# Performance work log

Measured on AMD Instinct MI355X. Metric: run time of the kernel, lower is better.

Reference implementation:

```python
import jax, jax.numpy as jnp
import numpy as np

B, T, D, H = 4, 2048, 1024, 16
HD = D // H

def setup_inputs() -> dict:
    key = jax.random.key(0)
    ks = jax.random.split(key, 12)
    s = 0.02
    return {
        "query": jax.random.normal(ks[0], (B, T, D), dtype=jnp.float32),
        "key_": jax.random.normal(ks[1], (B, T, D), dtype=jnp.float32),
        "value": jax.random.normal(ks[2], (B, T, D), dtype=jnp.float32),
        "attention_mask": jnp.zeros((B, T, T), dtype=bool),
        "Wq": jax.random.normal(ks[3], (D, D), dtype=jnp.float32) * s,
        "bq": jnp.zeros((D,), dtype=jnp.float32),
        "Wk": jax.random.normal(ks[4], (D, D), dtype=jnp.float32) * s,
        "bk": jnp.zeros((D,), dtype=jnp.float32),
        "Wv": jax.random.normal(ks[5], (D, D), dtype=jnp.float32) * s,
        "bv": jnp.zeros((D,), dtype=jnp.float32),
        "Wo": jax.random.normal(ks[6], (D, D), dtype=jnp.float32) * s,
        "bo": jnp.zeros((D,), dtype=jnp.float32),
    }

def reference(query, key_, value, attention_mask, Wq, bq, Wk, bk, Wv, bv, Wo, bo):
    scale = 1.0 / jnp.sqrt(jnp.float32(HD))
    # projections (torch Linear: x @ W.T + b), split heads -> [B, H, T, HD]
    q = (query @ Wq.T + bq).reshape(B, T, H, HD).transpose(0, 2, 1, 3)
    k = (key_ @ Wk.T + bk).reshape(B, T, H, HD).transpose(0, 2, 1, 3)
    v = (value @ Wv.T + bv).reshape(B, T, H, HD).transpose(0, 2, 1, 3)
    scores = jnp.einsum('bhqd,bhkd->bhqk', q, k) * scale  # [B,H,T,T]
    mask = attention_mask[:, None, :, :]  # [B,1,T,T], True = masked
    scores = jnp.where(mask, -jnp.inf, scores)
    attn = jax.nn.softmax(scores, axis=-1)
    out = jnp.einsum('bhqk,bhkd->bhqd', attn, v)  # [B,H,T,HD]
    out = out.transpose(0, 2, 1, 3).reshape(B, T, D)
    return out @ Wo.T + bo
```

## Files before the change

kernel.cpp:

```cpp
#include <hip/hip_runtime.h>
#include <hip/hip_bf16.h>
#include <math.h>


typedef short bf16x8 __attribute__((ext_vector_type(8)));
typedef short bf16x4 __attribute__((ext_vector_type(4)));
typedef float f32x4  __attribute__((ext_vector_type(4)));
typedef float f32x16 __attribute__((ext_vector_type(16)));
typedef unsigned u32x4v __attribute__((ext_vector_type(4)));

#define DEV __device__ __forceinline__

DEV short f2bf(float f) {
    union { float f; unsigned u; } x; x.f = f;
    unsigned r = x.u + 0x7fffu + ((x.u >> 16) & 1u);
    return (short)(r >> 16);
}

DEV unsigned cvtpk(float lo, float hi) {
    unsigned r;
    asm("v_cvt_pk_bf16_f32 %0, %1, %2" : "=v"(r) : "v"(lo), "v"(hi));
    return r;
}

DEV void pl32swap(unsigned &a, unsigned &b) {
    asm volatile("v_permlane32_swap_b32 %0, %1" : "+v"(a), "+v"(b));
}

DEV float fexp2(float x) {
    float r;
    asm("v_exp_f32 %0, %1\n\ts_nop 0" : "=v"(r) : "v"(x));
    return r;
}

DEV void gload16(const void* g, void* lds_wave_base) {
    __builtin_amdgcn_global_load_lds(
        (const __attribute__((address_space(1))) void*)g,
        (__attribute__((address_space(3))) void*)lds_wave_base, 16, 0, 0);
}

DEV f32x4 mfma16(bf16x8 a, bf16x8 b, f32x4 c) {
    return __builtin_amdgcn_mfma_f32_16x16x32_bf16(a, b, c, 0, 0, 0);
}
DEV f32x16 mfma32(bf16x8 a, bf16x8 b, f32x16 c) {
    return __builtin_amdgcn_mfma_f32_32x32x16_bf16(a, b, c, 0, 0, 0);
}

__global__ __launch_bounds__(256) void cvt_w4(
    const float* __restrict__ a, const float* __restrict__ b,
    const float* __restrict__ c, const float* __restrict__ d,
    short* __restrict__ oa, short* __restrict__ ob,
    short* __restrict__ oc, short* __restrict__ od) {
    const int sel = blockIdx.x >> 9;
    const float* in = sel == 0 ? a : sel == 1 ? b : sel == 2 ? c : d;
    short* out      = sel == 0 ? oa : sel == 1 ? ob : sel == 2 ? oc : od;
    int i = ((blockIdx.x & 511) * 256 + threadIdx.x) * 8;
    f32x4 x = *(const f32x4*)(in + i);
    f32x4 y = *(const f32x4*)(in + i + 4);
    union { unsigned u[4]; bf16x8 v; } p;
    p.u[0] = cvtpk(x[0], x[1]); p.u[1] = cvtpk(x[2], x[3]);
    p.u[2] = cvtpk(y[0], y[1]); p.u[3] = cvtpk(y[2], y[3]);
    *(bf16x8*)(out + i) = p.v;
}

__global__ __launch_bounds__(256) void gemm_qkv(
    const float* __restrict__ Aq, const float* __restrict__ Ak, const float* __restrict__ Av,
    const short* __restrict__ Wqb, const short* __restrict__ Wkb, const short* __restrict__ Wvb,
    const float* __restrict__ bqp, const float* __restrict__ bkp, const float* __restrict__ bvp,
    short* __restrict__ Qo, short* __restrict__ Ko, short* __restrict__ Vo, float qscale)
{
    __shared__ short Alds[2][4096];
    __shared__ short Blds[2][4096];

    const int t = threadIdx.x, wave = t >> 6, lane = t & 63;
    const int lr = lane & 15, lg = lane >> 4;
    const int raw = blockIdx.x;
    const int wg = (raw & 7) * 192 + (raw >> 3);
    const int sel = wg >> 9, inner = wg & 511;
    const int m0 = (inner >> 3) * 128, n0 = (inner & 7) * 128;
    const int wr = wave >> 1, wc = wave & 1;

    const float* A    = sel == 0 ? Aq  : sel == 1 ? Ak  : Av;
    const short* W    = sel == 0 ? Wqb : sel == 1 ? Wkb : Wvb;
    const float* bias = sel == 0 ? bqp : sel == 1 ? bkp : bvp;

    const int arow = t & 127, kh = t >> 7;
    const float* Asrc = A + (size_t)(m0 + arow) * 1024 + kh * 16;
    const int o0 = t * 16,        kb0 = o0 >> 11, row0 = (o0 >> 4) & 127;
    const int o1 = 4096 + t * 16, kb1 = o1 >> 11, row1 = (o1 >> 4) & 127;
    const short* Ws0 = W + (size_t)(n0 + row0) * 1024 + kb0 * 8;
    const short* Ws1 = W + (size_t)(n0 + row1) * 1024 + kb1 * 8;

    f32x4 ar0, ar1, ar2, ar3;
    auto aload = [&](int k0) {
        ar0 = *(const f32x4*)(Asrc + k0);
        ar1 = *(const f32x4*)(Asrc + k0 + 4);
        ar2 = *(const f32x4*)(Asrc + k0 + 8);
        ar3 = *(const f32x4*)(Asrc + k0 + 12);
    };
    auto awrite = [&](short* dst0) {
        union { unsigned u[4]; bf16x8 v; } p0, p1;
        p0.u[0] = cvtpk(ar0[0], ar0[1]); p0.u[1] = cvtpk(ar0[2], ar0[3]);
        p0.u[2] = cvtpk(ar1[0], ar1[1]); p0.u[3] = cvtpk(ar1[2], ar1[3]);
        p1.u[0] = cvtpk(ar2[0], ar2[1]); p1.u[1] = cvtpk(ar2[2], ar2[3]);
        p1.u[2] = cvtpk(ar3[0], ar3[1]); p1.u[3] = cvtpk(ar3[2], ar3[3]);
        short* dst = dst0 + (kh * 2) * 1024 + arow * 8;
        *(bf16x8*)dst          = p0.v;
        *(bf16x8*)(dst + 1024) = p1.v;
    };
    auto wstage = [&](short* dB, int k0) {
        gload16(Ws0 + k0, (char*)dB + wave * 1024);
        gload16(Ws1 + k0, (char*)dB + 4096 + wave * 1024);
    };

    f32x4 acc[4][4] = {};

    aload(0);
    asm volatile("s_waitcnt vmcnt(0)" ::: "memory");
    awrite(Alds[0]);
    wstage(Blds[0], 0);
    aload(32);

    #pragma unroll 1
    for (int ts = 0; ts < 32; ++ts) {
        const int B = ts & 1;
        if (ts < 31) asm volatile("s_waitcnt vmcnt(4) lgkmcnt(0)" ::: "memory");
        else         asm volatile("s_waitcnt vmcnt(0) lgkmcnt(0)" ::: "memory");
        __builtin_amdgcn_s_barrier();
        bf16x8 af[4], bfr[4];
        #pragma unroll
        for (int mi = 0; mi < 4; mi++)
            af[mi] = *(const bf16x8*)(Alds[B] + lg * 1024 + (wr * 64 + mi * 16 + lr) * 8);
        #pragma unroll
        for (int ni = 0; ni < 4; ni++)
            bfr[ni] = *(const bf16x8*)(Blds[B] + lg * 1024 + (wc * 64 + ni * 16 + lr) * 8);
        if (ts < 31) wstage(Blds[B ^ 1], (ts + 1) * 32);
        #pragma unroll
        for (int mi = 0; mi < 4; mi++)
            #pragma unroll
            for (int ni = 0; ni < 4; ni++)
                acc[mi][ni] = mfma16(af[mi], bfr[ni], acc[mi][ni]);
        if (ts < 31) {
            asm volatile("s_waitcnt vmcnt(2)" ::: "memory");
            awrite(Alds[B ^ 1]);
            if (ts < 30) aload((ts + 2) * 32);
        }
    }

    #pragma unroll
    for (int mi = 0; mi < 4; mi++) {
        #pragma unroll
        for (int ni = 0; ni < 4; ni++) {
            const int n      = n0 + wc * 64 + ni * 16 + lr;
            const int m_base = m0 + wr * 64 + mi * 16 + lg * 4;
            const float bv   = bias[n];
            f32x4 a = acc[mi][ni];
            if (sel == 2) {
                const int bb = m_base >> 11, tt = m_base & 2047;
                bf16x4 p;
                #pragma unroll
                for (int r = 0; r < 4; r++) p[r] = f2bf(a[r] + bv);
                *(bf16x4*)(Vo + (size_t)bb * 2097152 + (size_t)n * 2048 + tt) = p;
            } else {
                short* C = sel ? Ko : Qo;
                const float sc = sel ? 1.0f : qscale;
                #pragma unroll
                for (int r = 0; r < 4; r++)
                    C[(size_t)(m_base + r) * 1024 + n] = f2bf((a[r] + bv) * sc);
            }
        }
    }
}

__global__ __launch_bounds__(256) void gemm_out(
    const short* __restrict__ A, const short* __restrict__ W,
    const float* __restrict__ bias, float* __restrict__ C)
{
    __shared__ short Alds[2][4096];
    __shared__ short Blds[2][4096];

    const int t = threadIdx.x;
    const int wave = t >> 6, lane = t & 63;
    const int lr = lane & 15, lg = lane >> 4;
    const int wg = (blockIdx.x & 7) * 64 + (blockIdx.x >> 3);
    const int m0 = (wg >> 3) * 128, n0 = (wg & 7) * 128;
    const int wr = wave >> 1, wc = wave & 1;

    const int o0 = t * 16,        kb0 = o0 >> 11, row0 = (o0 >> 4) & 127;
    const int o1 = 4096 + t * 16, kb1 = o1 >> 11, row1 = (o1 >> 4) & 127;
    const short* As0 = A + (size_t)(m0 + row0) * 1024 + kb0 * 8;
    const short* As1 = A + (size_t)(m0 + row1) * 1024 + kb1 * 8;
    const short* Ws0 = W + (size_t)(n0 + row0) * 1024 + kb0 * 8;
    const short* Ws1 = W + (size_t)(n0 + row1) * 1024 + kb1 * 8;

    auto stage = [&](short* dA, short* dB, int k0) {
        gload16(As0 + k0, (char*)dA + wave * 1024);
        gload16(As1 + k0, (char*)dA + 4096 + wave * 1024);
        gload16(Ws0 + k0, (char*)dB + wave * 1024);
        gload16(Ws1 + k0, (char*)dB + 4096 + wave * 1024);
    };

    f32x4 acc[4][4] = {};
    stage(Alds[0], Blds[0], 0);

    auto kstep = [&](int ts, int BUF) {
        if (ts < 31) {
            stage(Alds[BUF ^ 1], Blds[BUF ^ 1], (ts + 1) * 32);
            asm volatile("s_waitcnt vmcnt(4)" ::: "memory");
        } else {
            asm volatile("s_waitcnt vmcnt(0)" ::: "memory");
        }
        __builtin_amdgcn_s_barrier();
        bf16x8 af[4], bfr[4];
        #pragma unroll
        for (int mi = 0; mi < 4; mi++)
            af[mi] = *(const bf16x8*)(Alds[BUF] + lg * 1024 + (wr * 64 + mi * 16 + lr) * 8);
        #pragma unroll
        for (int ni = 0; ni < 4; ni++)
            bfr[ni] = *(const bf16x8*)(Blds[BUF] + lg * 1024 + (wc * 64 + ni * 16 + lr) * 8);
        #pragma unroll
        for (int mi = 0; mi < 4; mi++)
            #pragma unroll
            for (int ni = 0; ni < 4; ni++)
                acc[mi][ni] = mfma16(af[mi], bfr[ni], acc[mi][ni]);
        __builtin_amdgcn_s_barrier();
    };

    #pragma unroll 1
    for (int it = 0; it < 16; ++it) { kstep(2 * it, 0); kstep(2 * it + 1, 1); }

    #pragma unroll
    for (int mi = 0; mi < 4; mi++) {
        #pragma unroll
        for (int ni = 0; ni < 4; ni++) {
            const int n      = n0 + wc * 64 + ni * 16 + lr;
            const int m_base = m0 + wr * 64 + mi * 16 + lg * 4;
            const float bv   = bias[n];
            f32x4 a = acc[mi][ni];
            #pragma unroll
            for (int r = 0; r < 4; r++)
                C[(size_t)(m_base + r) * 1024 + n] = a[r] + bv;
        }
    }
}

__global__ __launch_bounds__(256) void mask_scan(const unsigned char* __restrict__ mask,
                                                 unsigned char* __restrict__ flags) {
    __shared__ int anyk[32];
    const int t = threadIdx.x, kt = t & 31, g = t >> 5;
    const int b = blockIdx.x >> 6, qt = blockIdx.x & 63;
    if (t < 32) anyk[t] = 0;
    __syncthreads();
    unsigned acc = 0;
    const unsigned char* base = mask + ((size_t)b * 2048 + qt * 32 + g * 4) * 2048 + kt * 64;
    #pragma unroll
    for (int rr = 0; rr < 4; rr++) {
        const uint4* p = (const uint4*)(base + (size_t)rr * 2048);
        #pragma unroll
        for (int s = 0; s < 4; s++) { uint4 v = p[s]; acc |= v.x | v.y | v.z | v.w; }
    }
    if (acc) anyk[kt] = 1;
    __syncthreads();
    if (t < 32) flags[((size_t)b * 64 + qt) * 32 + t] = (unsigned char)anyk[t];
}

__global__ __launch_bounds__(256, 2) void attn_fwd3(
    const short* __restrict__ Q, const short* __restrict__ K,
    const short* __restrict__ Vt, const unsigned char* __restrict__ mask,
    const unsigned char* __restrict__ flags, short* __restrict__ O)
{
    __shared__ short lds[2][2][8192];

    const int t = threadIdx.x, wave = t >> 6, lane = t & 63;
    const int j31 = lane & 31, hi = lane >> 5;

    const int raw = blockIdx.x;
    const int wg  = (raw & 7) * 128 + (raw >> 3);
    const int qblk = wg & 15, bh = wg >> 4;
    const int h = bh & 15, b = bh >> 4;
    const int q0 = qblk * 128 + wave * 32;

    bf16x8 qf[4];
    {
        const short* qp = Q + ((size_t)b * 2048 + q0 + j31) * 1024 + h * 64 + hi * 8;
        #pragma unroll
        for (int ck = 0; ck < 4; ck++) qf[ck] = *(const bf16x8*)(qp + ck * 16);
    }
    unsigned long long fmask;
    {
        unsigned char fb = flags[((size_t)b * 64 + qblk * 4 + wave) * 32 + j31];
        fmask = __ballot(fb != 0);
    }
    bf16x8 onesv;
    #pragma unroll
    for (int i = 0; i < 8; i++) onesv[i] = (short)0x3F80;

    const short* Kg = K + ((size_t)b * 2048) * 1024 + h * 64;
    const short* Vg = Vt + (size_t)b * 2097152 + (size_t)h * 64 * 2048;

    auto stage = [&](short* dK, short* dV, int tk) {
        #pragma unroll
        for (int i = 0; i < 4; i++) {
            const int s = i * 256 + t;
            const int rK = s >> 3, cK = ((s & 7) ^ (rK & 7)) * 8;
            gload16(Kg + (size_t)(tk + rK) * 1024 + cK, dK + i * 2048 + wave * 512);
            const int rV = s >> 4, cV = ((s & 15) ^ (rV & 15)) * 8;
            gload16(Vg + (size_t)rV * 2048 + tk + cV, dV + i * 2048 + wave * 512);
        }
    };

    stage(&lds[0][0][0], &lds[0][1][0], 0);

    f32x16 oA = {}, oB = {}, accL = {};
    float m = -1e30f;
    const int swk = j31 & 7, swv = j31 & 15;

    auto tile = [&](int J, int BUF) {
        if (J < 15) {
            stage(&lds[BUF ^ 1][0][0], &lds[BUF ^ 1][1][0], (J + 1) * 128);
            asm volatile("s_waitcnt vmcnt(8)" ::: "memory");
        } else {
            asm volatile("s_waitcnt vmcnt(0)" ::: "memory");
        }
        __builtin_amdgcn_s_barrier();
        const short* ldsK = &lds[BUF][0][0];
        const short* ldsV = &lds[BUF][1][0];

        f32x16 sA = {}, sB = {}, sC = {}, sD = {};
        __builtin_amdgcn_s_setprio(1);
        #pragma unroll
        for (int ck = 0; ck < 4; ck++) {
            const int co = ((2 * ck + hi) ^ swk) * 8;
            bf16x8 k0 = *(const bf16x8*)(ldsK + (j31      ) * 64 + co);
            bf16x8 k1 = *(const bf16x8*)(ldsK + (32 + j31) * 64 + co);
            bf16x8 k2 = *(const bf16x8*)(ldsK + (64 + j31) * 64 + co);
            bf16x8 k3 = *(const bf16x8*)(ldsK + (96 + j31) * 64 + co);
            sA = mfma32(k0, qf[ck], sA);
            sB = mfma32(k1, qf[ck], sB);
            sC = mfma32(k2, qf[ck], sC);
            sD = mfma32(k3, qf[ck], sD);
        }
        __builtin_amdgcn_s_setprio(0);

        if ((fmask >> (2 * J)) & 3ULL) {
            const unsigned char* mp = mask + ((size_t)b * 2048 + q0 + j31) * 2048
                                           + (size_t)J * 128 + hi * 4;
            auto apply = [&](f32x16& sX, int X) {
                #pragma unroll
                for (int rg = 0; rg < 4; rg++) {
                    unsigned mb = *(const unsigned*)(mp + X * 32 + rg * 8);
                    #pragma unroll
                    for (int e = 0; e < 4; e++)
                        if ((mb >> (8 * e)) & 0xFFu) sX[rg * 4 + e] = -1e30f;
                }
            };
            apply(sA, 0); apply(sB, 1); apply(sC, 2); apply(sD, 3);
        }

        float tm = fmaxf(sA[0], sA[1]);
        #pragma unroll
        for (int r = 2; r < 16; r += 2) tm = fmaxf(fmaxf(tm, sA[r]), sA[r + 1]);
        #pragma unroll
        for (int r = 0; r < 16; r += 2) tm = fmaxf(fmaxf(tm, sB[r]), sB[r + 1]);
        #pragma unroll
        for (int r = 0; r < 16; r += 2) tm = fmaxf(fmaxf(tm, sC[r]), sC[r + 1]);
        #pragma unroll
        for (int r = 0; r < 16; r += 2) tm = fmaxf(fmaxf(tm, sD[r]), sD[r + 1]);
        tm = fmaxf(tm, __shfl_xor(tm, 32));
        if (!__all(tm <= m + 8.f)) {
            const float mnew = fmaxf(m, tm);
            const float fs = fexp2(m - mnew);
            m = mnew;
            #pragma unroll
            for (int r = 0; r < 16; r++) { oA[r] *= fs; oB[r] *= fs; }
            accL[0] *= fs;
        }
        #pragma unroll
        for (int r = 0; r < 16; r++) sA[r] = fexp2(sA[r] - m);
        #pragma unroll
        for (int r = 0; r < 16; r++) sB[r] = fexp2(sB[r] - m);
        #pragma unroll
        for (int r = 0; r < 16; r++) sC[r] = fexp2(sC[r] - m);
        #pragma unroll
        for (int r = 0; r < 16; r++) sD[r] = fexp2(sD[r] - m);

        __builtin_amdgcn_s_setprio(1);
        #pragma unroll
        for (int c = 0; c < 8; c++) {
            const f32x16& sX = (c < 2) ? sA : (c < 4) ? sB : (c < 6) ? sC : sD;
            const int rb = 8 * (c & 1);
            unsigned A0 = cvtpk(sX[rb],     sX[rb + 1]), B0 = cvtpk(sX[rb + 4], sX[rb + 5]);
            unsigned A1 = cvtpk(sX[rb + 2], sX[rb + 3]), B1 = cvtpk(sX[rb + 6], sX[rb + 7]);
            pl32swap(A0, B0); pl32swap(A1, B1);
            union { unsigned u[4]; bf16x8 v; } pu;
            pu.u[0] = A0; pu.u[1] = A1; pu.u[2] = B0; pu.u[3] = B1;
            const int co = ((2 * c + hi) ^ swv) * 8;
            bf16x8 v0 = *(const bf16x8*)(ldsV + (j31      ) * 128 + co);
            bf16x8 v1 = *(const bf16x8*)(ldsV + (32 + j31) * 128 + co);
            oA   = mfma32(v0, pu.v, oA);
            oB   = mfma32(v1, pu.v, oB);
            accL = mfma32(onesv, pu.v, accL);
        }
        __builtin_amdgcn_s_setprio(0);
        __builtin_amdgcn_s_barrier();
    };

    #pragma unroll 1
    for (int jj = 0; jj < 8; ++jj) { tile(2 * jj, 0); tile(2 * jj + 1, 1); }

    __syncthreads();
    unsigned* ow = (unsigned*)&lds[0][0][0] + wave * (32 * 34);
    const float inv = 1.f / accL[0];
    #pragma unroll
    for (int o = 0; o < 2; o++)
        #pragma unroll
        for (int rp = 0; rp < 8; rp++) {
            const int r  = 2 * rp;
            const int hd = 2 * (rp & 1) + 8 * (rp >> 1) + 4 * hi + 32 * o;
            const float v0 = (o ? oB[r]     : oA[r])     * inv;
            const float v1 = (o ? oB[r + 1] : oA[r + 1]) * inv;
            ow[j31 * 34 + (hd >> 1)] = cvtpk(v0, v1);
        }
    __syncthreads();
    {
        const size_t orow = ((size_t)b * 2048 + q0 + j31) * 1024 + h * 64 + hi * 32;
        unsigned* gout = (unsigned*)(O + orow);
        const unsigned* src = ow + j31 * 34 + hi * 16;
        #pragma unroll
        for (int i = 0; i < 4; i++) {
            u32x4v v;
            v[0] = src[i*4]; v[1] = src[i*4+1]; v[2] = src[i*4+2]; v[3] = src[i*4+3];
            *(u32x4v*)(gout + i * 4) = v;
        }
    }
}

extern "C" void kernel_launch(void* const* d_in, const int* in_sizes, int n_in,
                              void* d_out, int out_size, void* d_ws, size_t ws_size,
                              hipStream_t stream)
{
    const float* query = (const float*)d_in[0];
    const float* key_  = (const float*)d_in[1];
    const float* value = (const float*)d_in[2];
    const unsigned char* amask = (const unsigned char*)d_in[3];
    const float* Wq = (const float*)d_in[4];
    const float* bq = (const float*)d_in[5];
    const float* Wk = (const float*)d_in[6];
    const float* bk = (const float*)d_in[7];
    const float* Wv = (const float*)d_in[8];
    const float* bv = (const float*)d_in[9];
    const float* Wo = (const float*)d_in[10];
    const float* bo = (const float*)d_in[11];
    float* out = (float*)d_out;

    char* ws = (char*)d_ws;
    const size_t MB = 1024 * 1024;
    short* Wqb = (short*)(ws + 0 * MB);
    short* Wkb = (short*)(ws + 2 * MB);
    short* Wvb = (short*)(ws + 4 * MB);
    short* Wob = (short*)(ws + 6 * MB);
    short* Qb  = (short*)(ws + 8 * MB);
    short* Kb  = (short*)(ws + 24 * MB);
    short* Vtb = (short*)(ws + 40 * MB);
    short* Xb  = (short*)(ws + 56 * MB);
    unsigned char* flagsb = (unsigned char*)(ws + 0 * MB);

    cvt_w4<<<2048, 256, 0, stream>>>(Wq, Wk, Wv, Wo, Wqb, Wkb, Wvb, Wob);

    const float qscale = 0.125f * 1.44269504088896f;
    gemm_qkv<<<1536, 256, 0, stream>>>(query, key_, value, Wqb, Wkb, Wvb,
                                       bq, bk, bv, Qb, Kb, Vtb, qscale);

    mask_scan<<<256, 256, 0, stream>>>(amask, flagsb);

    attn_fwd3<<<1024, 256, 0, stream>>>(Qb, Kb, Vtb, amask, flagsb, Xb);

    gemm_out<<<512, 256, 0, stream>>>(Xb, Wob, bo, out);
}
```

Baseline: 289.6 us.

## Split fused QKV GEMM into separate activation conversion and bf16 GEMM launches

Replaces the fused QKV projection kernel, which loaded fp32 activations and converted them to bf16 in registers before writing LDS, with a standalone fp32-to-bf16 conversion pass followed by a templated bf16 GEMM. That GEMM stages both operands via direct global-to-LDS loads and is reused for Q, K, V and the output projection. The goal is to simplify the GEMM inner loop and let both operands use async LDS loads. The cost is six launches in place of one, an extra round trip of the activations through memory, and less parallelism per launch (512 blocks each rather than 1536).

After: 280.2 us. -3.2%, faster.

```diff
diff --git a/kernel.cpp b/kernel.cpp
--- a/kernel.cpp
+++ b/kernel.cpp
@@ -44,6 +44,17 @@
 }
 DEV f32x16 mfma32(bf16x8 a, bf16x8 b, f32x16 c) {
     return __builtin_amdgcn_mfma_f32_32x32x16_bf16(a, b, c, 0, 0, 0);
+}
+
+__global__ __launch_bounds__(256) void cvt_one(const float* __restrict__ in,
+                                               short* __restrict__ out) {
+    int i = (blockIdx.x * 256 + threadIdx.x) * 8;
+    f32x4 a = *(const f32x4*)(in + i);
+    f32x4 b = *(const f32x4*)(in + i + 4);
+    union { unsigned u[4]; bf16x8 v; } p;
+    p.u[0] = cvtpk(a[0], a[1]); p.u[1] = cvtpk(a[2], a[3]);
+    p.u[2] = cvtpk(b[0], b[1]); p.u[3] = cvtpk(b[2], b[3]);
+    *(bf16x8*)(out + i) = p.v;
 }
 
 __global__ __launch_bounds__(256) void cvt_w4(
@@ -63,118 +74,10 @@
     *(bf16x8*)(out + i) = p.v;
 }
 
-__global__ __launch_bounds__(256) void gemm_qkv(
-    const float* __restrict__ Aq, const float* __restrict__ Ak, const float* __restrict__ Av,
-    const short* __restrict__ Wqb, const short* __restrict__ Wkb, const short* __restrict__ Wvb,
-    const float* __restrict__ bqp, const float* __restrict__ bkp, const float* __restrict__ bvp,
-    short* __restrict__ Qo, short* __restrict__ Ko, short* __restrict__ Vo, float qscale)
-{
-    __shared__ short Alds[2][4096];
-    __shared__ short Blds[2][4096];
-
-    const int t = threadIdx.x, wave = t >> 6, lane = t & 63;
-    const int lr = lane & 15, lg = lane >> 4;
-    const int raw = blockIdx.x;
-    const int wg = (raw & 7) * 192 + (raw >> 3);
-    const int sel = wg >> 9, inner = wg & 511;
-    const int m0 = (inner >> 3) * 128, n0 = (inner & 7) * 128;
-    const int wr = wave >> 1, wc = wave & 1;
-
-    const float* A    = sel == 0 ? Aq  : sel == 1 ? Ak  : Av;
-    const short* W    = sel == 0 ? Wqb : sel == 1 ? Wkb : Wvb;
-    const float* bias = sel == 0 ? bqp : sel == 1 ? bkp : bvp;
-
-    const int arow = t & 127, kh = t >> 7;
-    const float* Asrc = A + (size_t)(m0 + arow) * 1024 + kh * 16;
-    const int o0 = t * 16,        kb0 = o0 >> 11, row0 = (o0 >> 4) & 127;
-    const int o1 = 4096 + t * 16, kb1 = o1 >> 11, row1 = (o1 >> 4) & 127;
-    const short* Ws0 = W + (size_t)(n0 + row0) * 1024 + kb0 * 8;
-    const short* Ws1 = W + (size_t)(n0 + row1) * 1024 + kb1 * 8;
-
-    f32x4 ar0, ar1, ar2, ar3;
-    auto aload = [&](int k0) {
-        ar0 = *(const f32x4*)(Asrc + k0);
-        ar1 = *(const f32x4*)(Asrc + k0 + 4);
-        ar2 = *(const f32x4*)(Asrc + k0 + 8);
-        ar3 = *(const f32x4*)(Asrc + k0 + 12);
-    };
-    auto awrite = [&](short* dst0) {
-        union { unsigned u[4]; bf16x8 v; } p0, p1;
-        p0.u[0] = cvtpk(ar0[0], ar0[1]); p0.u[1] = cvtpk(ar0[2], ar0[3]);
-        p0.u[2] = cvtpk(ar1[0], ar1[1]); p0.u[3] = cvtpk(ar1[2], ar1[3]);
-        p1.u[0] = cvtpk(ar2[0], ar2[1]); p1.u[1] = cvtpk(ar2[2], ar2[3]);
-        p1.u[2] = cvtpk(ar3[0], ar3[1]); p1.u[3] = cvtpk(ar3[2], ar3[3]);
-        short* dst = dst0 + (kh * 2) * 1024 + arow * 8;
-        *(bf16x8*)dst          = p0.v;
-        *(bf16x8*)(dst + 1024) = p1.v;
-    };
-    auto wstage = [&](short* dB, int k0) {
-        gload16(Ws0 + k0, (char*)dB + wave * 1024);
-        gload16(Ws1 + k0, (char*)dB + 4096 + wave * 1024);
-    };
-
-    f32x4 acc[4][4] = {};
-
-    aload(0);
-    asm volatile("s_waitcnt vmcnt(0)" ::: "memory");
-    awrite(Alds[0]);
-    wstage(Blds[0], 0);
-    aload(32);
-
-    #pragma unroll 1
-    for (int ts = 0; ts < 32; ++ts) {
-        const int B = ts & 1;
-        if (ts < 31) asm volatile("s_waitcnt vmcnt(4) lgkmcnt(0)" ::: "memory");
-        else         asm volatile("s_waitcnt vmcnt(0) lgkmcnt(0)" ::: "memory");
-        __builtin_amdgcn_s_barrier();
-        bf16x8 af[4], bfr[4];
-        #pragma unroll
-        for (int mi = 0; mi < 4; mi++)
-            af[mi] = *(const bf16x8*)(Alds[B] + lg * 1024 + (wr * 64 + mi * 16 + lr) * 8);
-        #pragma unroll
-        for (int ni = 0; ni < 4; ni++)
-            bfr[ni] = *(const bf16x8*)(Blds[B] + lg * 1024 + (wc * 64 + ni * 16 + lr) * 8);
-        if (ts < 31) wstage(Blds[B ^ 1], (ts + 1) * 32);
-        #pragma unroll
-        for (int mi = 0; mi < 4; mi++)
-            #pragma unroll
-            for (int ni = 0; ni < 4; ni++)
-                acc[mi][ni] = mfma16(af[mi], bfr[ni], acc[mi][ni]);
-        if (ts < 31) {
-            asm volatile("s_waitcnt vmcnt(2)" ::: "memory");
-            awrite(Alds[B ^ 1]);
-            if (ts < 30) aload((ts + 2) * 32);
-        }
-    }
-
-    #pragma unroll
-    for (int mi = 0; mi < 4; mi++) {
-        #pragma unroll
-        for (int ni = 0; ni < 4; ni++) {
-            const int n      = n0 + wc * 64 + ni * 16 + lr;
-            const int m_base = m0 + wr * 64 + mi * 16 + lg * 4;
-            const float bv   = bias[n];
-            f32x4 a = acc[mi][ni];
-            if (sel == 2) {
-                const int bb = m_base >> 11, tt = m_base & 2047;
-                bf16x4 p;
-                #pragma unroll
-                for (int r = 0; r < 4; r++) p[r] = f2bf(a[r] + bv);
-                *(bf16x4*)(Vo + (size_t)bb * 2097152 + (size_t)n * 2048 + tt) = p;
-            } else {
-                short* C = sel ? Ko : Qo;
-                const float sc = sel ? 1.0f : qscale;
-                #pragma unroll
-                for (int r = 0; r < 4; r++)
-                    C[(size_t)(m_base + r) * 1024 + n] = f2bf((a[r] + bv) * sc);
-            }
-        }
-    }
-}
-
-__global__ __launch_bounds__(256) void gemm_out(
+template<int EPI>
+__global__ __launch_bounds__(256) void gemm_bt(
     const short* __restrict__ A, const short* __restrict__ W,
-    const float* __restrict__ bias, float* __restrict__ C)
+    const float* __restrict__ bias, void* __restrict__ Cp, float epiScale)
 {
     __shared__ short Alds[2][4096];
     __shared__ short Blds[2][4096];
@@ -201,6 +104,7 @@
     };
 
     f32x4 acc[4][4] = {};
+
     stage(Alds[0], Blds[0], 0);
 
     auto kstep = [&](int ts, int BUF) {
@@ -237,9 +141,24 @@
             const int m_base = m0 + wr * 64 + mi * 16 + lg * 4;
             const float bv   = bias[n];
             f32x4 a = acc[mi][ni];
-            #pragma unroll
-            for (int r = 0; r < 4; r++)
-                C[(size_t)(m_base + r) * 1024 + n] = a[r] + bv;
+            if constexpr (EPI == 0) {
+                short* C = (short*)Cp;
+                #pragma unroll
+                for (int r = 0; r < 4; r++)
+                    C[(size_t)(m_base + r) * 1024 + n] = f2bf((a[r] + bv) * epiScale);
+            } else if constexpr (EPI == 2) {
+                short* C = (short*)Cp;
+                const int b = m_base >> 11, tt = m_base & 2047;
+                bf16x4 p;
+                #pragma unroll
+                for (int r = 0; r < 4; r++) p[r] = f2bf(a[r] + bv);
+                *(bf16x4*)(C + (size_t)b * 2097152 + (size_t)n * 2048 + tt) = p;
+            } else {
+                float* C = (float*)Cp;
+                #pragma unroll
+                for (int r = 0; r < 4; r++)
+                    C[(size_t)(m_base + r) * 1024 + n] = a[r] + bv;
+            }
         }
     }
 }
@@ -468,12 +387,16 @@
     cvt_w4<<<2048, 256, 0, stream>>>(Wq, Wk, Wv, Wo, Wqb, Wkb, Wvb, Wob);
 
     const float qscale = 0.125f * 1.44269504088896f;
-    gemm_qkv<<<1536, 256, 0, stream>>>(query, key_, value, Wqb, Wkb, Wvb,
-                                       bq, bk, bv, Qb, Kb, Vtb, qscale);
+    cvt_one<<<4096, 256, 0, stream>>>(query, Xb);
+    gemm_bt<0><<<512, 256, 0, stream>>>(Xb, Wqb, bq, Qb, qscale);
+    cvt_one<<<4096, 256, 0, stream>>>(key_, Xb);
+    gemm_bt<0><<<512, 256, 0, stream>>>(Xb, Wkb, bk, Kb, 1.0f);
+    cvt_one<<<4096, 256, 0, stream>>>(value, Xb);
+    gemm_bt<2><<<512, 256, 0, stream>>>(Xb, Wvb, bv, Vtb, 1.0f);
 
     mask_scan<<<256, 256, 0, stream>>>(amask, flagsb);
 
     attn_fwd3<<<1024, 256, 0, stream>>>(Qb, Kb, Vtb, amask, flagsb, Xb);
 
-    gemm_out<<<512, 256, 0, stream>>>(Xb, Wob, bo, out);
-}
+    gemm_bt<3><<<512, 256, 0, stream>>>(Xb, Wob, bo, out, 1.0f);
+}
```

## Stage fp32 activations directly to LDS and convert to bf16 at fragment load

Applied to the files above, without the earlier changes.

The QKV projection GEMM now copies the fp32 A tile straight from global memory into LDS with direct global-to-LDS loads, using a swizzled column-pair layout. The fp32-to-bf16 conversion moves from register staging before the LDS write to the fragment read out of LDS. The pipeline becomes issue-next-stage-then-wait with barriers on both sides of each k-step. This removes register staging and the VGPR pressure from held A loads, but doubles the A-tile LDS footprint and LDS read bandwidth, and repeats the conversion for each wave that reads the same data.

After: 257.9 us. 10.9% less time.

```diff
diff --git a/kernel.cpp b/kernel.cpp
--- a/kernel.cpp
+++ b/kernel.cpp
@@ -63,13 +63,13 @@
     *(bf16x8*)(out + i) = p.v;
 }
 
-__global__ __launch_bounds__(256) void gemm_qkv(
+__global__ __launch_bounds__(256) void gemm_qkv2(
     const float* __restrict__ Aq, const float* __restrict__ Ak, const float* __restrict__ Av,
     const short* __restrict__ Wqb, const short* __restrict__ Wkb, const short* __restrict__ Wvb,
     const float* __restrict__ bqp, const float* __restrict__ bkp, const float* __restrict__ bvp,
     short* __restrict__ Qo, short* __restrict__ Ko, short* __restrict__ Vo, float qscale)
 {
-    __shared__ short Alds[2][4096];
+    __shared__ float Alds[2][4096];
     __shared__ short Blds[2][4096];
 
     const int t = threadIdx.x, wave = t >> 6, lane = t & 63;
@@ -84,75 +84,75 @@
     const short* W    = sel == 0 ? Wqb : sel == 1 ? Wkb : Wvb;
     const float* bias = sel == 0 ? bqp : sel == 1 ? bkp : bvp;
 
-    const int arow = t & 127, kh = t >> 7;
-    const float* Asrc = A + (size_t)(m0 + arow) * 1024 + kh * 16;
+    const float* Asrc0; const float* Asrc1; const float* Asrc2; const float* Asrc3;
+    {
+        auto mk = [&](int i) {
+            const int p = i * 256 + t, kq = p >> 8, cp = p & 255;
+            const int rp = cp >> 1, pc = cp & 1, cpair = pc ^ ((rp >> 3) & 1);
+            return A + (size_t)(m0 + rp) * 1024 + kq * 8 + cpair * 4;
+        };
+        Asrc0 = mk(0); Asrc1 = mk(1); Asrc2 = mk(2); Asrc3 = mk(3);
+    }
     const int o0 = t * 16,        kb0 = o0 >> 11, row0 = (o0 >> 4) & 127;
     const int o1 = 4096 + t * 16, kb1 = o1 >> 11, row1 = (o1 >> 4) & 127;
     const short* Ws0 = W + (size_t)(n0 + row0) * 1024 + kb0 * 8;
     const short* Ws1 = W + (size_t)(n0 + row1) * 1024 + kb1 * 8;
 
-    f32x4 ar0, ar1, ar2, ar3;
-    auto aload = [&](int k0) {
-        ar0 = *(const f32x4*)(Asrc + k0);
-        ar1 = *(const f32x4*)(Asrc + k0 + 4);
-        ar2 = *(const f32x4*)(Asrc + k0 + 8);
-        ar3 = *(const f32x4*)(Asrc + k0 + 12);
-    };
-    auto awrite = [&](short* dst0) {
-        union { unsigned u[4]; bf16x8 v; } p0, p1;
-        p0.u[0] = cvtpk(ar0[0], ar0[1]); p0.u[1] = cvtpk(ar0[2], ar0[3]);
-        p0.u[2] = cvtpk(ar1[0], ar1[1]); p0.u[3] = cvtpk(ar1[2], ar1[3]);
-        p1.u[0] = cvtpk(ar2[0], ar2[1]); p1.u[1] = cvtpk(ar2[2], ar2[3]);
-        p1.u[2] = cvtpk(ar3[0], ar3[1]); p1.u[3] = cvtpk(ar3[2], ar3[3]);
-        short* dst = dst0 + (kh * 2) * 1024 + arow * 8;
-        *(bf16x8*)dst          = p0.v;
-        *(bf16x8*)(dst + 1024) = p1.v;
-    };
-    auto wstage = [&](short* dB, int k0) {
+    auto stage = [&](float* dA, short* dB, int k0) {
+        gload16(Asrc0 + k0, (char*)dA +         wave * 1024);
+        gload16(Asrc1 + k0, (char*)dA +  4096 + wave * 1024);
+        gload16(Asrc2 + k0, (char*)dA +  8192 + wave * 1024);
+        gload16(Asrc3 + k0, (char*)dA + 12288 + wave * 1024);
         gload16(Ws0 + k0, (char*)dB + wave * 1024);
         gload16(Ws1 + k0, (char*)dB + 4096 + wave * 1024);
     };
 
+    const int s16 = (lr >> 3) & 1;
+    const int aBase = lg * 1024 + (wr * 64 + lr) * 8;
+    const int loOff = aBase + s16 * 4;
+    const int hiOff = aBase + (s16 ^ 1) * 4;
+
     f32x4 acc[4][4] = {};
-
-    aload(0);
-    asm volatile("s_waitcnt vmcnt(0)" ::: "memory");
-    awrite(Alds[0]);
-    wstage(Blds[0], 0);
-    aload(32);
-
-    #pragma unroll 1
-    for (int ts = 0; ts < 32; ++ts) {
-        const int B = ts & 1;
-        if (ts < 31) asm volatile("s_waitcnt vmcnt(4) lgkmcnt(0)" ::: "memory");
-        else         asm volatile("s_waitcnt vmcnt(0) lgkmcnt(0)" ::: "memory");
+    stage(Alds[0], Blds[0], 0);
+
+    auto kstep = [&](int ts, int BUF) {
+        if (ts < 31) {
+            stage(Alds[BUF ^ 1], Blds[BUF ^ 1], (ts + 1) * 32);
+            asm volatile("s_waitcnt vmcnt(6)" ::: "memory");
+        } else {
+            asm volatile("s_waitcnt vmcnt(0)" ::: "memory");
+        }
         __builtin_amdgcn_s_barrier();
         bf16x8 af[4], bfr[4];
         #pragma unroll
-        for (int mi = 0; mi < 4; mi++)
-            af[mi] = *(const bf16x8*)(Alds[B] + lg * 1024 + (wr * 64 + mi * 16 + lr) * 8);
+        for (int mi = 0; mi < 4; mi++) {
+            f32x4 lo = *(const f32x4*)(&Alds[BUF][0] + loOff + mi * 128);
+            f32x4 hi = *(const f32x4*)(&Alds[BUF][0] + hiOff + mi * 128);
+            union { unsigned u[4]; bf16x8 v; } pa;
+            pa.u[0] = cvtpk(lo[0], lo[1]); pa.u[1] = cvtpk(lo[2], lo[3]);
+            pa.u[2] = cvtpk(hi[0], hi[1]); pa.u[3] = cvtpk(hi[2], hi[3]);
+            af[mi] = pa.v;
+        }
         #pragma unroll
         for (int ni = 0; ni < 4; ni++)
-            bfr[ni] = *(const bf16x8*)(Blds[B] + lg * 1024 + (wc * 64 + ni * 16 + lr) * 8);
-        if (ts < 31) wstage(Blds[B ^ 1], (ts + 1) * 32);
+            bfr[ni] = *(const bf16x8*)(&Blds[BUF][0] + lg * 1024 + (wc * 64 + ni * 16 + lr) * 8);
         #pragma unroll
         for (int mi = 0; mi < 4; mi++)
             #pragma unroll
             for (int ni = 0; ni < 4; ni++)
                 acc[mi][ni] = mfma16(af[mi], bfr[ni], acc[mi][ni]);
-        if (ts < 31) {
-            asm volatile("s_waitcnt vmcnt(2)" ::: "memory");
-            awrite(Alds[B ^ 1]);
-            if (ts < 30) aload((ts + 2) * 32);
-        }
-    }
+        __builtin_amdgcn_s_barrier();
+    };
+
+    #pragma unroll 1
+    for (int it = 0; it < 16; ++it) { kstep(2 * it, 0); kstep(2 * it + 1, 1); }
 
     #pragma unroll
     for (int mi = 0; mi < 4; mi++) {
         #pragma unroll
         for (int ni = 0; ni < 4; ni++) {
             const int n      = n0 + wc * 64 + ni * 16 + lr;
-            const int m_base = m0 + wr * 64 + mi * 16 + lg * 4;
+            const int m_base = m0 + wr * 64 + mi * 16 + (lane >> 4) * 4;
             const float bv   = bias[n];
             f32x4 a = acc[mi][ni];
             if (sel == 2) {
@@ -468,8 +468,8 @@
     cvt_w4<<<2048, 256, 0, stream>>>(Wq, Wk, Wv, Wo, Wqb, Wkb, Wvb, Wob);
 
     const float qscale = 0.125f * 1.44269504088896f;
-    gemm_qkv<<<1536, 256, 0, stream>>>(query, key_, value, Wqb, Wkb, Wvb,
-                                       bq, bk, bv, Qb, Kb, Vtb, qscale);
+    gemm_qkv2<<<1536, 256, 0, stream>>>(query, key_, value, Wqb, Wkb, Wvb,
+                                        bq, bk, bv, Qb, Kb, Vtb, qscale);
 
     mask_scan<<<256, 256, 0, stream>>>(amask, flagsb);
 
```
